# Kernel optimization log

Measured on AMD Instinct MI355X. Metric: run time of the kernel, lower is better.

## Reference

```python
import jax, jax.numpy as jnp
import numpy as np

HEADS = 8
DIM_HEAD = 32
DIM = 256           # must equal HEADS*DIM_HEAD (required by the torch view)
HIDDEN = HEADS * DIM_HEAD
NUM_GROUPS = 32
EPS = 1e-6


def setup_inputs() -> dict:
    key = jax.random.key(0)
    ks = jax.random.split(key, 6)
    b, c, h, w = 16, DIM, 64, 64
    x = jax.random.normal(ks[0], (b, c, h, w), dtype=jnp.float32)
    # conv1x1 weights stored as 2D matrices (out_ch, in_ch)
    w_qkv = jax.random.normal(ks[1], (3 * HIDDEN, DIM), dtype=jnp.float32) * (1.0 / np.sqrt(DIM))
    w_out = jax.random.normal(ks[2], (DIM, HIDDEN), dtype=jnp.float32) * (1.0 / np.sqrt(HIDDEN))
    b_out = jax.random.normal(ks[3], (DIM,), dtype=jnp.float32) * 0.01
    gn_gamma = jnp.ones((DIM,), dtype=jnp.float32)
    gn_beta = jnp.zeros((DIM,), dtype=jnp.float32)
    return {"x": x, "w_qkv": w_qkv, "w_out": w_out, "b_out": b_out,
            "gn_gamma": gn_gamma, "gn_beta": gn_beta}


def _group_norm(x, gamma, beta):
    # GroupNorm32: compute in float32, eps=1e-6, affine
    b, c, h, w = x.shape
    g = NUM_GROUPS
    xf = x.astype(jnp.float32).reshape(b, g, c // g, h, w)
    mean = xf.mean(axis=(2, 3, 4), keepdims=True)
    var = xf.var(axis=(2, 3, 4), keepdims=True)
    xn = (xf - mean) * jax.lax.rsqrt(var + EPS)
    xn = xn.reshape(b, c, h, w)
    return (xn * gamma[None, :, None, None] + beta[None, :, None, None]).astype(x.dtype)


def reference(x, w_qkv, w_out, b_out, gn_gamma, gn_beta):
    b, c, h, w = x.shape
    n = h * w
    # qkv projection (1x1 conv == matmul over channels)
    qkv = jnp.einsum('oc,bchw->bohw', w_qkv, x)            # (b, 3*hidden, h, w)
    qkv = qkv.reshape(b, 3, HEADS, DIM_HEAD, n)
    q, k, v = qkv[:, 0], qkv[:, 1], qkv[:, 2]              # (b, h, d, n)
    q = jax.nn.softmax(q, axis=-2)                         # softmax over feature dim
    k = jax.nn.softmax(k, axis=-1)                         # softmax over spatial dim
    context = jnp.einsum('bhdn,bhen->bhde', k, v)          # (b, heads, d, d)
    out = jnp.einsum('bhde,bhdn->bhen', context, q)        # (b, heads, d, n)
    out = out.reshape(b, c, h, w)
    out = jnp.einsum('oc,bchw->bohw', w_out, out) + b_out[None, :, None, None]
    out = _group_norm(out, gn_gamma, gn_beta)
    return out + x
```

## Files before the change

kernel.cpp:

```cpp
#include <hip/hip_runtime.h>


typedef short s8v __attribute__((ext_vector_type(8)));
typedef float f32x4 __attribute__((ext_vector_type(4)));

__device__ __forceinline__ short f2bf(float f) {
  union { float f; unsigned u; } v; v.f = f;
  unsigned r = v.u + 0x7FFF + ((v.u >> 16) & 1);
  return (short)(r >> 16);
}
__device__ __forceinline__ float bf2f(short h) {
  union { unsigned u; float f; } v; v.u = ((unsigned)(unsigned short)h) << 16;
  return v.f;
}
__device__ __forceinline__ void gld16(const short* g, short* l) {
  __builtin_amdgcn_global_load_lds(
      (const __attribute__((address_space(1))) unsigned*)g,
      (__attribute__((address_space(3))) unsigned*)l, 16, 0, 0);
}

__global__ __launch_bounds__(256) void cast_w(
    const float* __restrict__ src, short* __restrict__ dst, float* __restrict__ st2) {
  if (blockIdx.x == 96) {
    float4 z = {0.f, 0.f, 0.f, 0.f};
    ((float4*)st2)[threadIdx.x] = z;
    return;
  }
  int id = blockIdx.x * 256 + threadIdx.x;
  long off = (long)id * 8;
  float4 a = *(const float4*)&src[off];
  float4 b = *(const float4*)&src[off + 4];
  s8v o;
  o[0] = f2bf(a.x); o[1] = f2bf(a.y); o[2] = f2bf(a.z); o[3] = f2bf(a.w);
  o[4] = f2bf(b.x); o[5] = f2bf(b.y); o[6] = f2bf(b.z); o[7] = f2bf(b.w);
  *(s8v*)&dst[off] = o;
}

__global__ __launch_bounds__(256) void cast_transpose_x(
    const float* __restrict__ x, short* __restrict__ xt) {
  int b = blockIdx.z;
  int n0 = blockIdx.x * 64, c0 = blockIdx.y * 64;
  __shared__ short ls[64][65];
  int t = threadIdx.x;
  const float* xb = x + ((long)b * 256 + c0) * 4096 + n0;
  int ci = t >> 4, j4 = (t & 15) * 4;
#pragma unroll
  for (int i = 0; i < 4; ++i) {
    int cl = ci + i * 16;
    float4 v = *(const float4*)&xb[(long)cl * 4096 + j4];
    ls[j4 + 0][cl] = f2bf(v.x);
    ls[j4 + 1][cl] = f2bf(v.y);
    ls[j4 + 2][cl] = f2bf(v.z);
    ls[j4 + 3][cl] = f2bf(v.w);
  }
  __syncthreads();
  short* xtb = xt + ((long)b * 4096 + n0) * 256 + c0;
#pragma unroll
  for (int i = 0; i < 2; ++i) {
    int id = t + i * 256;
    int nl = id >> 3, c8 = (id & 7) * 8;
    s8v o;
#pragma unroll
    for (int e = 0; e < 8; ++e) o[e] = ls[nl][c8 + e];
    *(s8v*)&xtb[(long)nl * 256 + c8] = o;
  }
}

__global__ __launch_bounds__(256) void gemm_qkv(
    const short* __restrict__ A, const short* __restrict__ Bt,
    short* __restrict__ kv, short* __restrict__ qT) {
  __shared__ short lA[8192];
  __shared__ short lB[8192];
  int b = blockIdx.z;
  int mt = blockIdx.y * 128, nt = blockIdx.x * 128;
  int tid = threadIdx.x;
  int lane = tid & 63;
  int wm = tid >> 7, wn = (tid >> 6) & 1;
  int rl = lane & 15, kg = lane >> 4;
  const short* Ab = A + (long)mt * 256;
  const short* Bb = Bt + ((long)b * 4096 + nt) * 256;

  f32x4 acc[4][4];
#pragma unroll
  for (int i = 0; i < 4; ++i)
#pragma unroll
    for (int j = 0; j < 4; ++j) acc[i][j] = (f32x4){0.f, 0.f, 0.f, 0.f};

  for (int k0 = 0; k0 < 256; k0 += 64) {
#pragma unroll
    for (int is = 0; is < 4; ++is) {
      int s = is * 256 + tid;
      int row = s >> 3, kcp = s & 7;
      int kcl = kcp ^ (row & 7);
      gld16(Ab + (long)row * 256 + k0 + kcl * 8, &lA[(is * 256 + (tid & ~63)) * 8]);
      gld16(Bb + (long)row * 256 + k0 + kcl * 8, &lB[(is * 256 + (tid & ~63)) * 8]);
    }
    asm volatile("s_waitcnt vmcnt(0)" ::: "memory");
    __syncthreads();
#pragma unroll
    for (int kw = 0; kw < 2; ++kw) {
      int kc = kw * 4 + kg;
      s8v av[4], bv[4];
#pragma unroll
      for (int mi = 0; mi < 4; ++mi) {
        int row = wm * 64 + mi * 16 + rl;
        av[mi] = *(const s8v*)&lA[row * 64 + ((kc ^ (row & 7)) << 3)];
      }
#pragma unroll
      for (int ni = 0; ni < 4; ++ni) {
        int row = wn * 64 + ni * 16 + rl;
        bv[ni] = *(const s8v*)&lB[row * 64 + ((kc ^ (row & 7)) << 3)];
      }
#pragma unroll
      for (int mi = 0; mi < 4; ++mi)
#pragma unroll
        for (int ni = 0; ni < 4; ++ni)
          acc[mi][ni] = __builtin_amdgcn_mfma_f32_16x16x32_bf16(
              av[mi], bv[ni], acc[mi][ni], 0, 0, 0);
    }
    __syncthreads();
  }

  if (mt < 256) {
    short* qTb = qT + ((long)b * 4096 + nt) * 256 + mt;
#pragma unroll
    for (int ni = 0; ni < 4; ++ni) {
      int n = wn * 64 + ni * 16 + rl;
#pragma unroll
      for (int p = 0; p < 2; ++p) {
        float v[8];
        float m = -1e30f;
#pragma unroll
        for (int j = 0; j < 8; ++j) {
          v[j] = acc[p * 2 + (j >> 2)][ni][j & 3];
          m = fmaxf(m, v[j]);
        }
        m = fmaxf(m, __shfl_xor(m, 16));
        m = fmaxf(m, __shfl_xor(m, 32));
        float ssum = 0.f;
#pragma unroll
        for (int j = 0; j < 8; ++j) { v[j] = __expf(v[j] - m); ssum += v[j]; }
        ssum += __shfl_xor(ssum, 16);
        ssum += __shfl_xor(ssum, 32);
        float inv = 1.f / ssum;
#pragma unroll
        for (int half = 0; half < 2; ++half) {
          short4 o;
          o.x = f2bf(v[half * 4 + 0] * inv);
          o.y = f2bf(v[half * 4 + 1] * inv);
          o.z = f2bf(v[half * 4 + 2] * inv);
          o.w = f2bf(v[half * 4 + 3] * inv);
          *(short4*)&qTb[(long)n * 256 + wm * 64 + p * 32 + half * 16 + kg * 4] = o;
        }
      }
    }
  } else {
    short* Cb = kv + ((long)b * 512 + (mt - 256)) * 4096 + nt;
#pragma unroll
    for (int mi = 0; mi < 4; ++mi) {
#pragma unroll
      for (int r = 0; r < 4; ++r) {
        int o = wm * 64 + mi * 16 + kg * 4 + r;
#pragma unroll
        for (int ni = 0; ni < 4; ++ni) {
          int n = wn * 64 + ni * 16 + rl;
          Cb[(long)o * 4096 + n] = f2bf(acc[mi][ni][r]);
        }
      }
    }
  }
}

__global__ __launch_bounds__(256) void gemm_lin(
    const short* __restrict__ A, const short* __restrict__ Bt,
    short* __restrict__ C, const float* __restrict__ bias,
    float* __restrict__ st2) {
  __shared__ short lA[8192];
  __shared__ short lB[8192];
  int b = blockIdx.z;
  int mt = blockIdx.y * 128, nt = blockIdx.x * 128;
  int tid = threadIdx.x;
  int lane = tid & 63;
  int wm = tid >> 7, wn = (tid >> 6) & 1;
  int rl = lane & 15, kg = lane >> 4;
  const short* Ab = A + (long)b * 65536 + (long)mt * 256;
  const short* Bb = Bt + ((long)b * 4096 + nt) * 256;

  f32x4 acc[4][4];
#pragma unroll
  for (int i = 0; i < 4; ++i)
#pragma unroll
    for (int j = 0; j < 4; ++j) acc[i][j] = (f32x4){0.f, 0.f, 0.f, 0.f};

  for (int k0 = 0; k0 < 256; k0 += 64) {
#pragma unroll
    for (int is = 0; is < 4; ++is) {
      int s = is * 256 + tid;
      int row = s >> 3, kcp = s & 7;
      int kcl = kcp ^ (row & 7);
      gld16(Ab + (long)row * 256 + k0 + kcl * 8, &lA[(is * 256 + (tid & ~63)) * 8]);
      gld16(Bb + (long)row * 256 + k0 + kcl * 8, &lB[(is * 256 + (tid & ~63)) * 8]);
    }
    asm volatile("s_waitcnt vmcnt(0)" ::: "memory");
    __syncthreads();
#pragma unroll
    for (int kw = 0; kw < 2; ++kw) {
      int kc = kw * 4 + kg;
      s8v av[4], bv[4];
#pragma unroll
      for (int mi = 0; mi < 4; ++mi) {
        int row = wm * 64 + mi * 16 + rl;
        av[mi] = *(const s8v*)&lA[row * 64 + ((kc ^ (row & 7)) << 3)];
      }
#pragma unroll
      for (int ni = 0; ni < 4; ++ni) {
        int row = wn * 64 + ni * 16 + rl;
        bv[ni] = *(const s8v*)&lB[row * 64 + ((kc ^ (row & 7)) << 3)];
      }
#pragma unroll
      for (int mi = 0; mi < 4; ++mi)
#pragma unroll
        for (int ni = 0; ni < 4; ++ni)
          acc[mi][ni] = __builtin_amdgcn_mfma_f32_16x16x32_bf16(
              av[mi], bv[ni], acc[mi][ni], 0, 0, 0);
    }
    __syncthreads();
  }

  short* Cb = C + ((long)b * 256 + mt) * 4096 + nt;
  float s1[4] = {0.f, 0.f, 0.f, 0.f};
  float s2[4] = {0.f, 0.f, 0.f, 0.f};
#pragma unroll
  for (int mi = 0; mi < 4; ++mi) {
#pragma unroll
    for (int r = 0; r < 4; ++r) {
      int o = wm * 64 + mi * 16 + kg * 4 + r;
      float bv = bias[mt + o];
#pragma unroll
      for (int ni = 0; ni < 4; ++ni) {
        int n = wn * 64 + ni * 16 + rl;
        short h = f2bf(acc[mi][ni][r] + bv);
        Cb[(long)o * 4096 + n] = h;
        float q = bf2f(h);
        s1[mi] += q;
        s2[mi] += q * q;
      }
    }
  }
#pragma unroll
  for (int mi = 0; mi < 4; ++mi) {
#pragma unroll
    for (int off = 1; off <= 16; off <<= 1) {
      s1[mi] += __shfl_xor(s1[mi], off);
      s2[mi] += __shfl_xor(s2[mi], off);
    }
    if (rl == 0 && (kg & 1) == 0) {
      int g = (mt >> 3) + wm * 8 + mi * 2 + (kg >> 1);
      atomicAdd(&st2[(b * 32 + g) * 2], s1[mi]);
      atomicAdd(&st2[(b * 32 + g) * 2 + 1], s2[mi]);
    }
  }
}

__global__ __launch_bounds__(256) void ctx_mfma(
    const short* __restrict__ kv, float* __restrict__ ctxp, float* __restrict__ sp) {
  int split = blockIdx.x;
  int h = blockIdx.y, b = blockIdx.z;
  int tid = threadIdx.x;
  int w = tid >> 6, l = tid & 63;
  const short* kb = kv + ((long)(b * 512) + h * 32) * 4096;
  const short* vb = kb + (long)256 * 4096;
  int rl = l & 15, kg = l >> 4;
  int n_base = split * 1024 + w * 256;

  f32x4 acc[2][2];
#pragma unroll
  for (int i = 0; i < 2; ++i)
#pragma unroll
    for (int j = 0; j < 2; ++j) acc[i][j] = (f32x4){0.f, 0.f, 0.f, 0.f};
  float s_part0 = 0.f, s_part1 = 0.f;

#pragma unroll 2
  for (int it = 0; it < 8; ++it) {
    int n0 = n_base + it * 32 + kg * 8;
    s8v a0, a1, b0, b1;
    {
      s8v kr = *(const s8v*)&kb[(long)rl * 4096 + n0];
#pragma unroll
      for (int j = 0; j < 8; ++j) {
        float f = __expf(bf2f(kr[j]));
        s_part0 += f;
        a0[j] = f2bf(f);
      }
    }
    {
      s8v kr = *(const s8v*)&kb[(long)(16 + rl) * 4096 + n0];
#pragma unroll
      for (int j = 0; j < 8; ++j) {
        float f = __expf(bf2f(kr[j]));
        s_part1 += f;
        a1[j] = f2bf(f);
      }
    }
    b0 = *(const s8v*)&vb[(long)rl * 4096 + n0];
    b1 = *(const s8v*)&vb[(long)(16 + rl) * 4096 + n0];
    acc[0][0] = __builtin_amdgcn_mfma_f32_16x16x32_bf16(a0, b0, acc[0][0], 0, 0, 0);
    acc[0][1] = __builtin_amdgcn_mfma_f32_16x16x32_bf16(a0, b1, acc[0][1], 0, 0, 0);
    acc[1][0] = __builtin_amdgcn_mfma_f32_16x16x32_bf16(a1, b0, acc[1][0], 0, 0, 0);
    acc[1][1] = __builtin_amdgcn_mfma_f32_16x16x32_bf16(a1, b1, acc[1][1], 0, 0, 0);
  }
  s_part0 += __shfl_xor(s_part0, 16); s_part0 += __shfl_xor(s_part0, 32);
  s_part1 += __shfl_xor(s_part1, 16); s_part1 += __shfl_xor(s_part1, 32);

  __shared__ float lctx[4][1024];
  __shared__ float lsum[4][32];
#pragma unroll
  for (int di = 0; di < 2; ++di)
#pragma unroll
    for (int ei = 0; ei < 2; ++ei)
#pragma unroll
      for (int r = 0; r < 4; ++r) {
        int row = di * 16 + kg * 4 + r;
        int col = ei * 16 + rl;
        lctx[w][row * 32 + col] = acc[di][ei][r];
      }
  if (kg == 0) { lsum[w][rl] = s_part0; lsum[w][16 + rl] = s_part1; }
  __syncthreads();
  long base = (long)(b * 8 + h) * 4 + split;
#pragma unroll
  for (int i = 0; i < 4; ++i) {
    int id = tid + i * 256;
    ctxp[base * 1024 + id] = lctx[0][id] + lctx[1][id] + lctx[2][id] + lctx[3][id];
  }
  if (tid < 32)
    sp[base * 32 + tid] = lsum[0][tid] + lsum[1][tid] + lsum[2][tid] + lsum[3][tid];
}

__global__ __launch_bounds__(256) void make_wf(
    const float* __restrict__ ctxp, const float* __restrict__ sp,
    const float* __restrict__ w_out, short* __restrict__ wf) {
  int h = blockIdx.x, b = blockIdx.y;
  __shared__ float c[32][33];
  __shared__ float inv_s[32];
  __shared__ float wv[256][33];
  int t = threadIdx.x;
  long base = (long)(b * 8 + h) * 4;
#pragma unroll
  for (int i = 0; i < 4; ++i) {
    int id = t + i * 256;
    float v = ctxp[base * 1024 + id] + ctxp[(base + 1) * 1024 + id] +
              ctxp[(base + 2) * 1024 + id] + ctxp[(base + 3) * 1024 + id];
    c[id >> 5][id & 31] = v;
  }
  if (t < 32) {
    float sv = sp[base * 32 + t] + sp[(base + 1) * 32 + t] +
               sp[(base + 2) * 32 + t] + sp[(base + 3) * 32 + t];
    inv_s[t] = 1.f / sv;
  }
#pragma unroll
  for (int r = 0; r < 32; ++r) {
    int row = r * 8 + (t >> 5);
    wv[row][t & 31] = w_out[row * 256 + h * 32 + (t & 31)];
  }
  __syncthreads();
  float wr[32];
#pragma unroll
  for (int e = 0; e < 32; ++e) wr[e] = wv[t][e];
  float tmp[32];
#pragma unroll
  for (int dd = 0; dd < 32; ++dd) {
    float sum = 0.f;
#pragma unroll
    for (int e = 0; e < 32; ++e) sum += wr[e] * c[dd][e];
    tmp[dd] = sum * inv_s[dd];
  }
  short* dst = wf + ((long)b * 256 + t) * 256 + h * 32;
#pragma unroll
  for (int c8 = 0; c8 < 4; ++c8) {
    s8v o;
#pragma unroll
    for (int e = 0; e < 8; ++e) o[e] = f2bf(tmp[c8 * 8 + e]);
    *(s8v*)&dst[c8 * 8] = o;
  }
}

__global__ __launch_bounds__(256) void final_out(
    const short* __restrict__ lin, const float* __restrict__ x,
    const float2* __restrict__ st2, const float* __restrict__ gamma,
    const float* __restrict__ beta, float* __restrict__ out) {
  long id = (long)blockIdx.x * 256 + threadIdx.x;
  long e0 = id * 8;
  int b = (int)(e0 >> 20);
  int rem = (int)(e0 & 1048575);
  int c = rem >> 12;
  float2 st = st2[b * 32 + (c >> 3)];
  float mean = st.x * (1.f / 32768.f);
  float inv = rsqrtf(st.y * (1.f / 32768.f) - mean * mean + 1e-6f);
  float ga = gamma[c] * inv;
  float be = beta[c] - mean * ga;
  s8v l8 = *(const s8v*)&lin[e0];
  float4 x0 = *(const float4*)&x[e0];
  float4 x1 = *(const float4*)&x[e0 + 4];
  float4 o0, o1;
  o0.x = bf2f(l8[0]) * ga + be + x0.x;
  o0.y = bf2f(l8[1]) * ga + be + x0.y;
  o0.z = bf2f(l8[2]) * ga + be + x0.z;
  o0.w = bf2f(l8[3]) * ga + be + x0.w;
  o1.x = bf2f(l8[4]) * ga + be + x1.x;
  o1.y = bf2f(l8[5]) * ga + be + x1.y;
  o1.z = bf2f(l8[6]) * ga + be + x1.z;
  o1.w = bf2f(l8[7]) * ga + be + x1.w;
  *(float4*)&out[e0] = o0;
  *(float4*)&out[e0 + 4] = o1;
}

extern "C" void kernel_launch(void* const* d_in, const int* in_sizes, int n_in,
                              void* d_out, int out_size, void* d_ws, size_t ws_size,
                              hipStream_t stream) {
  const float* x     = (const float*)d_in[0];
  const float* w_qkv = (const float*)d_in[1];
  const float* w_out = (const float*)d_in[2];
  const float* b_out = (const float*)d_in[3];
  const float* gamma = (const float*)d_in[4];
  const float* beta  = (const float*)d_in[5];
  float* out = (float*)d_out;

  short* xt   = (short*)d_ws;
  short* qT   = xt + 16777216;
  short* kvb  = qT + 16777216;
  short* lin  = kvb + 33554432;
  short* wqb  = lin + 16777216;
  short* wfb  = wqb + 196608;
  float* ctxp = (float*)(wfb + 1048576);
  float* sp   = ctxp + 524288;
  float* st2  = sp + 16384;

  cast_w<<<97, 256, 0, stream>>>(w_qkv, wqb, st2);
  cast_transpose_x<<<dim3(64, 4, 16), 256, 0, stream>>>(x, xt);
  gemm_qkv<<<dim3(32, 6, 16), 256, 0, stream>>>(wqb, xt, kvb, qT);
  ctx_mfma<<<dim3(4, 8, 16), 256, 0, stream>>>(kvb, ctxp, sp);
  make_wf<<<dim3(8, 16), 256, 0, stream>>>(ctxp, sp, w_out, wfb);
  gemm_lin<<<dim3(32, 2, 16), 256, 0, stream>>>(wfb, qT, lin, b_out, st2);
  final_out<<<8192, 256, 0, stream>>>(lin, x, (const float2*)st2, gamma, beta, out);
}
```

Measured before the change: 149.8 us.

## Fuse k/v context reduction into QKV GEMM epilogue via LDS and atomics

The K/V tiles of the QKV GEMM are regrouped so that each block holds the K and V rows for two heads. In the epilogue it exponentiates K, stages both in LDS, and computes the partial context with MFMA, accumulating it and the softmax sums into global buffers with atomics. This removes the bf16 K/V write to global memory, the separate ctx_mfma kernel and the split-partial reduction in make_wf. The cost is many float atomics on contended addresses (ctxp and sp zeroed by extra cast_w blocks) and non-deterministic summation order. The exp is applied without max subtraction, the same as before.

Result: slower. 180.5 us (+20.5%).

```diff
diff --git a/kernel.cpp b/kernel.cpp
--- a/kernel.cpp
+++ b/kernel.cpp
@@ -20,13 +20,15 @@
 }
 
 __global__ __launch_bounds__(256) void cast_w(
-    const float* __restrict__ src, short* __restrict__ dst, float* __restrict__ st2) {
-  if (blockIdx.x == 96) {
+    const float* __restrict__ src, short* __restrict__ dst, float* __restrict__ zbase) {
+  int bx = blockIdx.x;
+  if (bx >= 96) {
+    int idx = (bx - 96) * 256 + threadIdx.x;
     float4 z = {0.f, 0.f, 0.f, 0.f};
-    ((float4*)st2)[threadIdx.x] = z;
+    ((float4*)zbase)[idx] = z;
     return;
   }
-  int id = blockIdx.x * 256 + threadIdx.x;
+  int id = bx * 256 + threadIdx.x;
   long off = (long)id * 8;
   float4 a = *(const float4*)&src[off];
   float4 b = *(const float4*)&src[off + 4];
@@ -68,16 +70,19 @@
 
 __global__ __launch_bounds__(256) void gemm_qkv(
     const short* __restrict__ A, const short* __restrict__ Bt,
-    short* __restrict__ kv, short* __restrict__ qT) {
-  __shared__ short lA[8192];
-  __shared__ short lB[8192];
+    short* __restrict__ qT, float* __restrict__ ctxp, float* __restrict__ sp) {
+  __shared__ short smem[16384];
+  short* lA = smem;
+  short* lB = smem + 8192;
   int b = blockIdx.z;
   int mt = blockIdx.y * 128, nt = blockIdx.x * 128;
+  bool isq = mt < 256;
+  int r = (mt - 256) >> 7;
+  int kbase = 256 + r * 64;
   int tid = threadIdx.x;
   int lane = tid & 63;
   int wm = tid >> 7, wn = (tid >> 6) & 1;
   int rl = lane & 15, kg = lane >> 4;
-  const short* Ab = A + (long)mt * 256;
   const short* Bb = Bt + ((long)b * 4096 + nt) * 256;
 
   f32x4 acc[4][4];
@@ -92,7 +97,8 @@
       int s = is * 256 + tid;
       int row = s >> 3, kcp = s & 7;
       int kcl = kcp ^ (row & 7);
-      gld16(Ab + (long)row * 256 + k0 + kcl * 8, &lA[(is * 256 + (tid & ~63)) * 8]);
+      int grow = isq ? (mt + row) : (kbase + row + ((row >= 64) ? 192 : 0));
+      gld16(A + (long)grow * 256 + k0 + kcl * 8, &lA[(is * 256 + (tid & ~63)) * 8]);
       gld16(Bb + (long)row * 256 + k0 + kcl * 8, &lB[(is * 256 + (tid & ~63)) * 8]);
     }
     asm volatile("s_waitcnt vmcnt(0)" ::: "memory");
@@ -121,7 +127,7 @@
     __syncthreads();
   }
 
-  if (mt < 256) {
+  if (isq) {
     short* qTb = qT + ((long)b * 4096 + nt) * 256 + mt;
 #pragma unroll
     for (int ni = 0; ni < 4; ++ni) {
@@ -155,19 +161,67 @@
       }
     }
   } else {
-    short* Cb = kv + ((long)b * 512 + (mt - 256)) * 4096 + nt;
+    int h2 = 2 * r;
 #pragma unroll
     for (int mi = 0; mi < 4; ++mi) {
 #pragma unroll
-      for (int r = 0; r < 4; ++r) {
-        int o = wm * 64 + mi * 16 + kg * 4 + r;
+      for (int rr = 0; rr < 4; ++rr) {
+        int rowl = mi * 16 + kg * 4 + rr;
+        float rs = 0.f;
 #pragma unroll
         for (int ni = 0; ni < 4; ++ni) {
-          int n = wn * 64 + ni * 16 + rl;
-          Cb[(long)o * 4096 + n] = f2bf(acc[mi][ni][r]);
+          int col = wn * 64 + ni * 16 + rl;
+          float val = acc[mi][ni][rr];
+          if (wm == 0) { val = __expf(val); rs += val; }
+          int phys = (((col >> 3) ^ (rowl & 7)) << 3) | (col & 7);
+          smem[(wm * 64 + rowl) * 128 + phys] = f2bf(val);
         }
-      }
-    }
+        if (wm == 0) {
+          rs += __shfl_xor(rs, 1); rs += __shfl_xor(rs, 2);
+          rs += __shfl_xor(rs, 4); rs += __shfl_xor(rs, 8);
+          if (rl == 0)
+            atomicAdd(&sp[((long)b * 8 + h2 + (rowl >> 5)) * 32 + (rowl & 31)], rs);
+        }
+      }
+    }
+    __syncthreads();
+    int w = tid >> 6;
+    int hh = w & 1, nh = w >> 1;
+    f32x4 c2[2][2];
+#pragma unroll
+    for (int i = 0; i < 2; ++i)
+#pragma unroll
+      for (int j = 0; j < 2; ++j) c2[i][j] = (f32x4){0.f, 0.f, 0.f, 0.f};
+#pragma unroll
+    for (int ks = 0; ks < 2; ++ks) {
+      int col = nh * 64 + ks * 32 + kg * 8;
+      int chunk = col >> 3;
+      s8v ka[2], va[2];
+#pragma unroll
+      for (int mi = 0; mi < 2; ++mi) {
+        int rowk = hh * 32 + mi * 16 + rl;
+        int rowv = 64 + hh * 32 + mi * 16 + rl;
+        ka[mi] = *(const s8v*)&smem[rowk * 128 + ((chunk ^ (rowk & 7)) << 3)];
+        va[mi] = *(const s8v*)&smem[rowv * 128 + ((chunk ^ (rowv & 7)) << 3)];
+      }
+#pragma unroll
+      for (int di = 0; di < 2; ++di)
+#pragma unroll
+        for (int ei = 0; ei < 2; ++ei)
+          c2[di][ei] = __builtin_amdgcn_mfma_f32_16x16x32_bf16(
+              ka[di], va[ei], c2[di][ei], 0, 0, 0);
+    }
+    float* cbase = ctxp + ((long)b * 8 + h2 + hh) * 1024;
+#pragma unroll
+    for (int di = 0; di < 2; ++di)
+#pragma unroll
+      for (int ei = 0; ei < 2; ++ei)
+#pragma unroll
+        for (int rr = 0; rr < 4; ++rr) {
+          int d = di * 16 + kg * 4 + rr;
+          int e = ei * 16 + rl;
+          atomicAdd(&cbase[d * 32 + e], c2[di][ei][rr]);
+        }
   }
 }
 
@@ -262,80 +316,6 @@
   }
 }
 
-__global__ __launch_bounds__(256) void ctx_mfma(
-    const short* __restrict__ kv, float* __restrict__ ctxp, float* __restrict__ sp) {
-  int split = blockIdx.x;
-  int h = blockIdx.y, b = blockIdx.z;
-  int tid = threadIdx.x;
-  int w = tid >> 6, l = tid & 63;
-  const short* kb = kv + ((long)(b * 512) + h * 32) * 4096;
-  const short* vb = kb + (long)256 * 4096;
-  int rl = l & 15, kg = l >> 4;
-  int n_base = split * 1024 + w * 256;
-
-  f32x4 acc[2][2];
-#pragma unroll
-  for (int i = 0; i < 2; ++i)
-#pragma unroll
-    for (int j = 0; j < 2; ++j) acc[i][j] = (f32x4){0.f, 0.f, 0.f, 0.f};
-  float s_part0 = 0.f, s_part1 = 0.f;
-
-#pragma unroll 2
-  for (int it = 0; it < 8; ++it) {
-    int n0 = n_base + it * 32 + kg * 8;
-    s8v a0, a1, b0, b1;
-    {
-      s8v kr = *(const s8v*)&kb[(long)rl * 4096 + n0];
-#pragma unroll
-      for (int j = 0; j < 8; ++j) {
-        float f = __expf(bf2f(kr[j]));
-        s_part0 += f;
-        a0[j] = f2bf(f);
-      }
-    }
-    {
-      s8v kr = *(const s8v*)&kb[(long)(16 + rl) * 4096 + n0];
-#pragma unroll
-      for (int j = 0; j < 8; ++j) {
-        float f = __expf(bf2f(kr[j]));
-        s_part1 += f;
-        a1[j] = f2bf(f);
-      }
-    }
-    b0 = *(const s8v*)&vb[(long)rl * 4096 + n0];
-    b1 = *(const s8v*)&vb[(long)(16 + rl) * 4096 + n0];
-    acc[0][0] = __builtin_amdgcn_mfma_f32_16x16x32_bf16(a0, b0, acc[0][0], 0, 0, 0);
-    acc[0][1] = __builtin_amdgcn_mfma_f32_16x16x32_bf16(a0, b1, acc[0][1], 0, 0, 0);
-    acc[1][0] = __builtin_amdgcn_mfma_f32_16x16x32_bf16(a1, b0, acc[1][0], 0, 0, 0);
-    acc[1][1] = __builtin_amdgcn_mfma_f32_16x16x32_bf16(a1, b1, acc[1][1], 0, 0, 0);
-  }
-  s_part0 += __shfl_xor(s_part0, 16); s_part0 += __shfl_xor(s_part0, 32);
-  s_part1 += __shfl_xor(s_part1, 16); s_part1 += __shfl_xor(s_part1, 32);
-
-  __shared__ float lctx[4][1024];
-  __shared__ float lsum[4][32];
-#pragma unroll
-  for (int di = 0; di < 2; ++di)
-#pragma unroll
-    for (int ei = 0; ei < 2; ++ei)
-#pragma unroll
-      for (int r = 0; r < 4; ++r) {
-        int row = di * 16 + kg * 4 + r;
-        int col = ei * 16 + rl;
-        lctx[w][row * 32 + col] = acc[di][ei][r];
-      }
-  if (kg == 0) { lsum[w][rl] = s_part0; lsum[w][16 + rl] = s_part1; }
-  __syncthreads();
-  long base = (long)(b * 8 + h) * 4 + split;
-#pragma unroll
-  for (int i = 0; i < 4; ++i) {
-    int id = tid + i * 256;
-    ctxp[base * 1024 + id] = lctx[0][id] + lctx[1][id] + lctx[2][id] + lctx[3][id];
-  }
-  if (tid < 32)
-    sp[base * 32 + tid] = lsum[0][tid] + lsum[1][tid] + lsum[2][tid] + lsum[3][tid];
-}
-
 __global__ __launch_bounds__(256) void make_wf(
     const float* __restrict__ ctxp, const float* __restrict__ sp,
     const float* __restrict__ w_out, short* __restrict__ wf) {
@@ -344,19 +324,13 @@
   __shared__ float inv_s[32];
   __shared__ float wv[256][33];
   int t = threadIdx.x;
-  long base = (long)(b * 8 + h) * 4;
+  long base = (long)(b * 8 + h);
 #pragma unroll
   for (int i = 0; i < 4; ++i) {
     int id = t + i * 256;
-    float v = ctxp[base * 1024 + id] + ctxp[(base + 1) * 1024 + id] +
-              ctxp[(base + 2) * 1024 + id] + ctxp[(base + 3) * 1024 + id];
-    c[id >> 5][id & 31] = v;
-  }
-  if (t < 32) {
-    float sv = sp[base * 32 + t] + sp[(base + 1) * 32 + t] +
-               sp[(base + 2) * 32 + t] + sp[(base + 3) * 32 + t];
-    inv_s[t] = 1.f / sv;
-  }
+    c[id >> 5][id & 31] = ctxp[base * 1024 + id];
+  }
+  if (t < 32) inv_s[t] = 1.f / sp[base * 32 + t];
 #pragma unroll
   for (int r = 0; r < 32; ++r) {
     int row = r * 8 + (t >> 5);
@@ -427,18 +401,16 @@
 
   short* xt   = (short*)d_ws;
   short* qT   = xt + 16777216;
-  short* kvb  = qT + 16777216;
-  short* lin  = kvb + 33554432;
+  short* lin  = qT + 16777216;
   short* wqb  = lin + 16777216;
   short* wfb  = wqb + 196608;
   float* ctxp = (float*)(wfb + 1048576);
-  float* sp   = ctxp + 524288;
-  float* st2  = sp + 16384;
-
-  cast_w<<<97, 256, 0, stream>>>(w_qkv, wqb, st2);
+  float* sp   = ctxp + 131072;
+  float* st2  = sp + 4096;
+
+  cast_w<<<229, 256, 0, stream>>>(w_qkv, wqb, ctxp);
   cast_transpose_x<<<dim3(64, 4, 16), 256, 0, stream>>>(x, xt);
-  gemm_qkv<<<dim3(32, 6, 16), 256, 0, stream>>>(wqb, xt, kvb, qT);
-  ctx_mfma<<<dim3(4, 8, 16), 256, 0, stream>>>(kvb, ctxp, sp);
+  gemm_qkv<<<dim3(32, 6, 16), 256, 0, stream>>>(wqb, xt, qT, ctxp, sp);
   make_wf<<<dim3(8, 16), 256, 0, stream>>>(ctxp, sp, w_out, wfb);
   gemm_lin<<<dim3(32, 2, 16), 256, 0, stream>>>(wfb, qT, lin, b_out, st2);
   final_out<<<8192, 256, 0, stream>>>(lin, x, (const float2*)st2, gamma, beta, out);
```
